# Kernel optimization log

Measured on AMD Instinct MI355X. Metric: run time of the kernel, lower is better.

## Reference

```python
import jax, jax.numpy as jnp
import numpy as np

C = 256
B, H, W = 16, 64, 64
CQK = C // 8


def setup_inputs() -> dict:
    key = jax.random.key(0)
    ks = jax.random.split(key, 8)
    s = 0.02
    return {
        "x": jax.random.normal(ks[0], (B, C, H, W), dtype=jnp.float32),
        "Wq": jax.random.normal(ks[1], (CQK, C), dtype=jnp.float32) * s,
        "bq": jax.random.normal(ks[2], (CQK,), dtype=jnp.float32) * s,
        "Wk": jax.random.normal(ks[3], (CQK, C), dtype=jnp.float32) * s,
        "bk": jax.random.normal(ks[4], (CQK,), dtype=jnp.float32) * s,
        "Wv": jax.random.normal(ks[5], (C, C), dtype=jnp.float32) * s,
        "bv": jax.random.normal(ks[6], (C,), dtype=jnp.float32) * s,
        "gamma": jax.random.normal(ks[7], (1,), dtype=jnp.float32) * 0.1,
    }


def reference(x, Wq, bq, Wk, bk, Wv, bv, gamma):
    b, c, h, w = x.shape
    n = h * w
    xf = x.reshape(b, c, n)  # flatten spatial -> tokens
    # 1x1 convs are per-token linear maps over channels
    q = jnp.einsum('oc,bcn->bon', Wq, xf) + bq[None, :, None]  # [B, C/8, N]
    k = jnp.einsum('oc,bcn->bon', Wk, xf) + bk[None, :, None]  # [B, C/8, N]
    v = jnp.einsum('oc,bcn->bon', Wv, xf) + bv[None, :, None]  # [B, C,   N]
    attn = jnp.einsum('bdi,bdj->bij', q, k)        # [B, N, N] = Q^T K
    attn = jax.nn.softmax(attn, axis=2)            # softmax over keys
    out = jnp.einsum('bcj,bij->bci', v, attn)      # V @ attn^T -> [B, C, N]
    out = out.reshape(b, c, h, w)
    return gamma[0] * out + x
```

## Files before the change

### kernel.cpp

```cpp
#include <hip/hip_runtime.h>
#include <hip/hip_bf16.h>

#define BB   16
#define CCH  256
#define DQK  32
#define NTOK 4096

typedef __attribute__((ext_vector_type(8)))  short short8;
typedef __attribute__((ext_vector_type(4)))  float f32x4;
typedef __attribute__((ext_vector_type(16))) float f32x16;
typedef unsigned short u16t;
typedef unsigned int   u32t;
typedef long long      i64t;

__device__ __forceinline__ u16t f2bf(float f){
  u32t u = __builtin_bit_cast(u32t, f);
  u += 0x7FFFu + ((u >> 16) & 1u);
  return (u16t)(u >> 16);
}
__device__ __forceinline__ u32t pk2(float a, float b){
  return (u32t)f2bf(a) | ((u32t)f2bf(b) << 16);
}
__device__ __forceinline__ void lane32swap(u32t& a, u32t& b){
  asm("v_permlane32_swap_b32 %0, %1" : "+v"(a), "+v"(b));
}
__device__ __forceinline__ float swapadd(float x){
  u32t a = __builtin_bit_cast(u32t, x), b = a;
  lane32swap(a, b);
  return __builtin_bit_cast(float, a) + __builtin_bit_cast(float, b);
}
__device__ __forceinline__ void gload16(const void* g, void* l){
  __builtin_amdgcn_global_load_lds(
      (const __attribute__((address_space(1))) void*)g,
      (__attribute__((address_space(3))) void*)l, 16, 0, 0);
}
__device__ __forceinline__ f32x16 zero16(){
  f32x16 z;
  #pragma unroll
  for (int i = 0; i < 16; ++i) z[i] = 0.f;
  return z;
}
#define mfma32(A, B, C)  __builtin_amdgcn_mfma_f32_32x32x16_bf16((A), (B), (C), 0, 0, 0)
#define mfma8(A, B, C)   __builtin_amdgcn_mfma_f32_32x32x16_fp8_fp8((A), (B), (C), 0, 0, 0)
__device__ __forceinline__ u32t pack4fp8(float a, float b, float c, float d){
  int t = __builtin_amdgcn_cvt_pk_fp8_f32(a, b, 0, false);
  t = __builtin_amdgcn_cvt_pk_fp8_f32(c, d, t, true);
  return (u32t)t;
}
__device__ __forceinline__ unsigned char tofp8(float v){
  return (unsigned char)(__builtin_amdgcn_cvt_pk_fp8_f32(v, 0.f, 0, false) & 0xFF);
}

__global__ __launch_bounds__(256) void k_wconv(const float* __restrict__ Wq,
    const float* __restrict__ Wk, const float* __restrict__ Wv,
    u16t* __restrict__ o){
  const int base = (blockIdx.x * 256 + threadIdx.x) * 4;
  float4 v;
  if (base < 8192)        v = *(const float4*)(Wq + base);
  else if (base < 16384)  v = *(const float4*)(Wk + base - 8192);
  else                    v = *(const float4*)(Wv + base - 16384);
  *(uint2*)(o + base) = make_uint2(pk2(v.x, v.y), pk2(v.z, v.w));
}

__global__ __launch_bounds__(256) void k_proj(const float* __restrict__ x,
    const u16t* __restrict__ Wb,
    const float* __restrict__ bq, const float* __restrict__ bk,
    const float* __restrict__ bv,
    u16t* __restrict__ Q, u16t* __restrict__ K, unsigned char* __restrict__ V){
  __shared__ __align__(16) u16t xt[32 * 512];
  const int b = blockIdx.y, nb = blockIdx.x * 64;
  const int tid = threadIdx.x;
  const int w = tid >> 6, lane = tid & 63;
  const int lo = lane & 15, g = lane >> 4;

  const float* xb = x + (size_t)b * CCH * NTOK + nb;
  const int cg = tid >> 4, n0 = (tid & 15) * 4;
  #pragma unroll
  for (int rep = 0; rep < 16; ++rep){
    const int c = rep * 16 + cg;
    float4 v = *(const float4*)(xb + (size_t)c * NTOK + n0);
    const int chunkb = (n0 >> 4) * 8 + (c >> 5);
    const int fl = 16 * ((c >> 3) & 3);
    const int e = c & 7;
    xt[chunkb * 512 + ((n0 & 15) + 0 + fl) * 8 + e] = f2bf(v.x);
    xt[chunkb * 512 + ((n0 & 15) + 1 + fl) * 8 + e] = f2bf(v.y);
    xt[chunkb * 512 + ((n0 & 15) + 2 + fl) * 8 + e] = f2bf(v.z);
    xt[chunkb * 512 + ((n0 & 15) + 3 + fl) * 8 + e] = f2bf(v.w);
  }
  __syncthreads();

  #pragma unroll
  for (int ot = 0; ot < 5; ++ot){
    const u16t* Wrow; const float* bias; int ob; int mode;
    if (ot == 0){
      if (w < 2){ Wrow = Wb;        bias = bq; ob = w * 16;       mode = 0; }
      else      { Wrow = Wb + 8192; bias = bk; ob = (w - 2) * 16; mode = 1; }
    } else { Wrow = Wb + 16384; bias = bv; ob = (ot - 1) * 64 + w * 16; mode = 2; }
    const u16t* wp = Wrow + (size_t)(ob + lo) * CCH + g * 8;

    f32x4 acc[4];
    #pragma unroll
    for (int s = 0; s < 4; ++s) acc[s] = (f32x4){0.f, 0.f, 0.f, 0.f};
    #pragma unroll
    for (int kc = 0; kc < CCH; kc += 32){
      const short8 af = *(const short8*)(wp + kc);
      #pragma unroll
      for (int s = 0; s < 4; ++s){
        const short8 bf = *(const short8*)(xt + (s * 8 + (kc >> 5)) * 512 + lane * 8);
        acc[s] = __builtin_amdgcn_mfma_f32_16x16x32_bf16(af, bf, acc[s], 0, 0, 0);
      }
    }
    #pragma unroll
    for (int s = 0; s < 4; ++s){
      #pragma unroll
      for (int r = 0; r < 4; ++r){
        const int o = ob + 4 * g + r;
        const int n = nb + s * 16 + lo;
        float val = acc[s][r] + bias[o];
        if (mode == 0){
          val *= 1.44269504088896f;
          Q[((size_t)b * NTOK + n) * DQK + o] = f2bf(val);
        } else if (mode == 1){
          K[((size_t)b * NTOK + n) * DQK + o] = f2bf(val);
        } else {
          const int swz = ((((s * 2) + (lo >> 3)) ^ ((o >> 1) & 7)) << 3) + (lo & 7);
          V[((size_t)b * CCH + o) * (size_t)NTOK + nb + swz] = tofp8(val);
        }
      }
    }
  }
}

__global__ __launch_bounds__(512, 4) void k_attn(
    const u16t* __restrict__ Q, const u16t* __restrict__ K,
    const unsigned char* __restrict__ V,
    const float* __restrict__ x, const float* __restrict__ gamma,
    float* __restrict__ out){
  __shared__ __align__(16) u16t KT[2 * 2048];
  __shared__ __align__(16) unsigned char Vt[2][16384];
  __shared__ __align__(16) unsigned char PT[2][8192];
  const int bid = blockIdx.x;
  const int b  = ((bid & 7) << 1) | ((bid >> 3) & 1);
  const int qt = bid >> 4;
  const int tid = threadIdx.x, w = tid >> 6, lane = tid & 63;
  const int qg = w & 3, ch = w >> 2;
  const int ql = lane & 31, hi = lane >> 5;
  const int qgb = qt * 128 + qg * 32;

  const u16t* Qb = Q + (size_t)b * NTOK * DQK;
  const u16t* Kb = K + (size_t)b * NTOK * DQK;
  const unsigned char* Vb = V + (size_t)b * CCH * NTOK;

  const short8 qf0 = *(const short8*)(Qb + (size_t)(qgb + ql) * DQK + hi * 8);
  const short8 qf1 = *(const short8*)(Qb + (size_t)(qgb + ql) * DQK + 16 + hi * 8);

  f32x16 acc[4];
  #pragma unroll
  for (int c = 0; c < 4; ++c) acc[c] = zero16();
  float l = 0.f;

  const char* vsrc0 = (const char*)Vb + (size_t)(w * 32 + (lane >> 2)) * NTOK + (lane & 3) * 16;
  const size_t kse = (size_t)((w & 1) * 32 + ql) * DQK + (w >> 1) * 16 + hi * 8;
  const char* ksrc0 = (const char*)Kb + kse * 2;
  const int kla = lane * 16;
  int vadd[4];
  #pragma unroll
  for (int kt = 0; kt < 4; ++kt)
    vadd[kt] = (ch * 128 + ql) * 64 + (((kt * 2 + hi) ^ ((ql >> 1) & 7)) << 3);
  const char* ldsV = (const char*)&Vt[0][0];
  const char* ldsK = (const char*)&KT[0];
  const char* ldsP = (const char*)&PT[0][0];
  char* ldsPw = (char*)&PT[0][0] + qg * 2048 + (ch * 2) * 512 + lane * 8;

  #define ESL(S, B) \
    { S[(B)+0] = __builtin_amdgcn_exp2f(S[(B)+0]); r0 += S[(B)+0]; \
      S[(B)+1] = __builtin_amdgcn_exp2f(S[(B)+1]); r1 += S[(B)+1]; \
      S[(B)+2] = __builtin_amdgcn_exp2f(S[(B)+2]); r2 += S[(B)+2]; \
      S[(B)+3] = __builtin_amdgcn_exp2f(S[(B)+3]); r3 += S[(B)+3]; }

  #define PVCHUNK(CS, VRD, EXPSLICE) \
    { const i64t vf0 = *(const i64t*)(ldsV + vadd[0] + (VRD)*16384 + (CS)*2048); \
      const i64t vf1 = *(const i64t*)(ldsV + vadd[1] + (VRD)*16384 + (CS)*2048); \
      const i64t vf2 = *(const i64t*)(ldsV + vadd[2] + (VRD)*16384 + (CS)*2048); \
      const i64t vf3 = *(const i64t*)(ldsV + vadd[3] + (VRD)*16384 + (CS)*2048); \
      acc[CS] = mfma8(vf0, pb0, acc[CS]); \
      acc[CS] = mfma8(vf1, pb1, acc[CS]); \
      acc[CS] = mfma8(vf2, pb2, acc[CS]); \
      acc[CS] = mfma8(vf3, pb3, acc[CS]); \
      EXPSLICE \
      __builtin_amdgcn_sched_group_barrier(0x100, 4, 0); \
      __builtin_amdgcn_sched_group_barrier(0x8,   4, 0); \
      __builtin_amdgcn_sched_group_barrier(0x2,   8, 0); }

  #define NOSL
  #define PBREADS(VRD) \
      const i64t pb0 = *(const i64t*)(ldsP + (VRD)*8192 + qg*2048 + 0*512 + lane*8); \
      const i64t pb1 = *(const i64t*)(ldsP + (VRD)*8192 + qg*2048 + 1*512 + lane*8); \
      const i64t pb2 = *(const i64t*)(ldsP + (VRD)*8192 + qg*2048 + 2*512 + lane*8); \
      const i64t pb3 = *(const i64t*)(ldsP + (VRD)*8192 + qg*2048 + 3*512 + lane*8);

  #define QKH(KRD, S) \
      { const char* kb_ = ldsK + (KRD)*4096 + ch*1024 + kla; \
        const short8 kfA = *(const short8*)(kb_); \
        const short8 kfB = *(const short8*)(kb_ + 2048); \
        S = mfma32(kfA, qf0, zero16()); \
        S = mfma32(kfB, qf1, S); }

  #define PWRITE(S, WB) \
      { u32t A1 = pack4fp8(S[0], S[1], S[2],  S[3]); \
        u32t B1 = pack4fp8(S[4], S[5], S[6],  S[7]); \
        lane32swap(A1, B1); \
        u32t A2 = pack4fp8(S[8], S[9], S[10], S[11]); \
        u32t B2 = pack4fp8(S[12], S[13], S[14], S[15]); \
        lane32swap(A2, B2); \
        *(i64t*)(ldsPw + (WB)*8192)       = __builtin_bit_cast(i64t, make_uint2(A1, B1)); \
        *(i64t*)(ldsPw + (WB)*8192 + 512) = __builtin_bit_cast(i64t, make_uint2(A2, B2)); }

  #define ABODY(T, VRD, KRD, KST) { \
      const int toff_ = ((T) + 1) * 64; \
      gload16(vsrc0 + toff_,                     &Vt[(VRD)^1][w * 2048]); \
      gload16(vsrc0 + (size_t)16 * NTOK + toff_, &Vt[(VRD)^1][w * 2048 + 1024]); \
      if (w < 4){ const int kt2_ = ((T) + 2 <= 63) ? (T) + 2 : 63; \
        gload16(ksrc0 + (size_t)kt2_ * 4096, &KT[(KST) * 2048 + w * 512]); } \
      PBREADS(VRD) \
      f32x16 s; \
      QKH(KRD, s) \
      float r0 = 0.f, r1 = 0.f, r2 = 0.f, r3 = 0.f; \
      PVCHUNK(0, VRD, ESL(s, 0)) \
      PVCHUNK(1, VRD, ESL(s, 4)) \
      PVCHUNK(2, VRD, ESL(s, 8)) \
      PVCHUNK(3, VRD, ESL(s, 12)) \
      l += (r0 + r1) + (r2 + r3); \
      PWRITE(s, (VRD)^1) \
      __syncthreads(); }

  gload16(vsrc0,                     &Vt[0][w * 2048]);
  gload16(vsrc0 + (size_t)16 * NTOK, &Vt[0][w * 2048 + 1024]);
  if (w < 4){
    gload16(ksrc0,        &KT[0 * 2048 + w * 512]);
    gload16(ksrc0 + 4096, &KT[1 * 2048 + w * 512]);
  }
  __syncthreads();

  {
    f32x16 s;
    QKH(0, s)
    float r0 = 0.f, r1 = 0.f, r2 = 0.f, r3 = 0.f;
    ESL(s, 0) ESL(s, 4) ESL(s, 8) ESL(s, 12)
    l = (r0 + r1) + (r2 + r3);
    PWRITE(s, 0)
  }
  __syncthreads();

  for (int t = 0; t < 62; t += 2){
    ABODY(t,     0, 1, 0)
    ABODY(t + 1, 1, 0, 1)
  }
  ABODY(62, 0, 1, 0)

  {
    PBREADS(1)
    PVCHUNK(0, 1, NOSL) PVCHUNK(1, 1, NOSL)
    PVCHUNK(2, 1, NOSL) PVCHUNK(3, 1, NOSL)
  }

  __syncthreads();
  const float lhalf = swapadd(l);
  float* lx = (float*)&PT[0][0];
  if (lane < 32) lx[(qg * 2 + ch) * 32 + ql] = lhalf;
  __syncthreads();
  const float lfull = lhalf + lx[(qg * 2 + (ch ^ 1)) * 32 + ql];
  const float inv = 1.0f / lfull;
  const float gm = gamma[0];
  const int n = qgb + ql;
  #pragma unroll
  for (int cs = 0; cs < 4; ++cs){
    #pragma unroll
    for (int r = 0; r < 16; ++r){
      const int c = ch * 128 + cs * 32 + (r & 3) + 8 * (r >> 2) + 4 * hi;
      const size_t idx = ((size_t)b * CCH + c) * NTOK + n;
      out[idx] = gm * (acc[cs][r] * inv) + x[idx];
    }
  }
  #undef ESL
  #undef PVCHUNK
  #undef NOSL
  #undef PBREADS
  #undef QKH
  #undef PWRITE
  #undef ABODY
}

extern "C" void kernel_launch(void* const* d_in, const int* in_sizes, int n_in,
                              void* d_out, int out_size, void* d_ws, size_t ws_size,
                              hipStream_t stream) {
  const float* x     = (const float*)d_in[0];
  const float* Wq    = (const float*)d_in[1];
  const float* bq    = (const float*)d_in[2];
  const float* Wk    = (const float*)d_in[3];
  const float* bk    = (const float*)d_in[4];
  const float* Wv    = (const float*)d_in[5];
  const float* bv    = (const float*)d_in[6];
  const float* gamma = (const float*)d_in[7];
  float* out = (float*)d_out;

  char* ws = (char*)d_ws;
  u16t* Qw = (u16t*)(ws);
  u16t* Kw = (u16t*)(ws + 4194304);
  unsigned char* Vw = (unsigned char*)(ws + 8388608);
  u16t* Wbf = (u16t*)d_out;

  hipLaunchKernelGGL(k_wconv, dim3(80), dim3(256), 0, stream, Wq, Wk, Wv, Wbf);
  hipLaunchKernelGGL(k_proj, dim3(NTOK / 64, BB), dim3(256), 0, stream,
                     x, Wbf, bq, bk, bv, Qw, Kw, Vw);
  hipLaunchKernelGGL(k_attn, dim3(512), dim3(512), 0, stream,
                     Qw, Kw, Vw, x, gamma, out);
}
```

Before: 163.6 us.

## Use 32x32x64 scaled MX fp8 MFMA for the PV product

Replaces four 32x32x16 fp8 MFMAs per channel chunk with one 32x32x64 scaled f8f6f4 MFMA, using unit scales. The V and P LDS read addressing and the P write layout are reworked to match the wider K-operand fragment, and the lane-swap shuffles in the P packing are dropped. The aim is to cut MFMA issue count and packing overhead in the attention inner loop. In exchange the P write/read pattern becomes 4-byte scattered accesses, which may cause more LDS traffic or bank conflicts.

```diff
diff --git a/kernel.cpp b/kernel.cpp
--- a/kernel.cpp
+++ b/kernel.cpp
@@ -7,6 +7,7 @@
 #define NTOK 4096
 
 typedef __attribute__((ext_vector_type(8)))  short short8;
+typedef __attribute__((ext_vector_type(8)))  int   i32x8;
 typedef __attribute__((ext_vector_type(4)))  float f32x4;
 typedef __attribute__((ext_vector_type(16))) float f32x16;
 typedef unsigned short u16t;
@@ -41,7 +42,7 @@
   return z;
 }
 #define mfma32(A, B, C)  __builtin_amdgcn_mfma_f32_32x32x16_bf16((A), (B), (C), 0, 0, 0)
-#define mfma8(A, B, C)   __builtin_amdgcn_mfma_f32_32x32x16_fp8_fp8((A), (B), (C), 0, 0, 0)
+#define mfmaMX(A, B, C)  __builtin_amdgcn_mfma_scale_f32_32x32x64_f8f6f4((A), (B), (C), 0, 0, 0, 127, 0, 127)
 __device__ __forceinline__ u32t pack4fp8(float a, float b, float c, float d){
   int t = __builtin_amdgcn_cvt_pk_fp8_f32(a, b, 0, false);
   t = __builtin_amdgcn_cvt_pk_fp8_f32(c, d, t, true);
@@ -163,14 +164,17 @@
   const size_t kse = (size_t)((w & 1) * 32 + ql) * DQK + (w >> 1) * 16 + hi * 8;
   const char* ksrc0 = (const char*)Kb + kse * 2;
   const int kla = lane * 16;
-  int vadd[4];
-  #pragma unroll
-  for (int kt = 0; kt < 4; ++kt)
-    vadd[kt] = (ch * 128 + ql) * 64 + (((kt * 2 + hi) ^ ((ql >> 1) & 7)) << 3);
+  int va[4];
+  #pragma unroll
+  for (int i = 0; i < 4; ++i){
+    const int c0 = ch * 128 + ql;
+    va[i] = (c0 & 127) * 64 + ch * 8192 + (((4 * hi + i) ^ ((c0 >> 1) & 7)) << 3);
+  }
   const char* ldsV = (const char*)&Vt[0][0];
   const char* ldsK = (const char*)&KT[0];
   const char* ldsP = (const char*)&PT[0][0];
-  char* ldsPw = (char*)&PT[0][0] + qg * 2048 + (ch * 2) * 512 + lane * 8;
+  char* ldsPw = (char*)&PT[0][0] + qg * 2048 + ch * 1024 + hi * 128 + ql * 4;
+  const int pread = qg * 2048 + hi * 1024 + ql * 4;
 
   #define ESL(S, B) \
     { S[(B)+0] = __builtin_amdgcn_exp2f(S[(B)+0]); r0 += S[(B)+0]; \
@@ -179,25 +183,25 @@
       S[(B)+3] = __builtin_amdgcn_exp2f(S[(B)+3]); r3 += S[(B)+3]; }
 
   #define PVCHUNK(CS, VRD, EXPSLICE) \
-    { const i64t vf0 = *(const i64t*)(ldsV + vadd[0] + (VRD)*16384 + (CS)*2048); \
-      const i64t vf1 = *(const i64t*)(ldsV + vadd[1] + (VRD)*16384 + (CS)*2048); \
-      const i64t vf2 = *(const i64t*)(ldsV + vadd[2] + (VRD)*16384 + (CS)*2048); \
-      const i64t vf3 = *(const i64t*)(ldsV + vadd[3] + (VRD)*16384 + (CS)*2048); \
-      acc[CS] = mfma8(vf0, pb0, acc[CS]); \
-      acc[CS] = mfma8(vf1, pb1, acc[CS]); \
-      acc[CS] = mfma8(vf2, pb2, acc[CS]); \
-      acc[CS] = mfma8(vf3, pb3, acc[CS]); \
+    { const uint2 v0 = *(const uint2*)(ldsV + va[0] + (VRD)*16384 + (CS)*2048); \
+      const uint2 v1 = *(const uint2*)(ldsV + va[1] + (VRD)*16384 + (CS)*2048); \
+      const uint2 v2 = *(const uint2*)(ldsV + va[2] + (VRD)*16384 + (CS)*2048); \
+      const uint2 v3 = *(const uint2*)(ldsV + va[3] + (VRD)*16384 + (CS)*2048); \
+      i32x8 av; \
+      av[0] = (int)v0.x; av[1] = (int)v0.y; av[2] = (int)v1.x; av[3] = (int)v1.y; \
+      av[4] = (int)v2.x; av[5] = (int)v2.y; av[6] = (int)v3.x; av[7] = (int)v3.y; \
+      acc[CS] = mfmaMX(av, pbv, acc[CS]); \
       EXPSLICE \
       __builtin_amdgcn_sched_group_barrier(0x100, 4, 0); \
-      __builtin_amdgcn_sched_group_barrier(0x8,   4, 0); \
+      __builtin_amdgcn_sched_group_barrier(0x8,   1, 0); \
       __builtin_amdgcn_sched_group_barrier(0x2,   8, 0); }
 
   #define NOSL
   #define PBREADS(VRD) \
-      const i64t pb0 = *(const i64t*)(ldsP + (VRD)*8192 + qg*2048 + 0*512 + lane*8); \
-      const i64t pb1 = *(const i64t*)(ldsP + (VRD)*8192 + qg*2048 + 1*512 + lane*8); \
-      const i64t pb2 = *(const i64t*)(ldsP + (VRD)*8192 + qg*2048 + 2*512 + lane*8); \
-      const i64t pb3 = *(const i64t*)(ldsP + (VRD)*8192 + qg*2048 + 3*512 + lane*8);
+      i32x8 pbv; \
+      _Pragma("unroll") \
+      for (int i_ = 0; i_ < 8; ++i_) \
+        pbv[i_] = *(const int*)(ldsP + (VRD)*8192 + pread + i_*128);
 
   #define QKH(KRD, S) \
       { const char* kb_ = ldsK + (KRD)*4096 + ch*1024 + kla; \
@@ -207,14 +211,10 @@
         S = mfma32(kfB, qf1, S); }
 
   #define PWRITE(S, WB) \
-      { u32t A1 = pack4fp8(S[0], S[1], S[2],  S[3]); \
-        u32t B1 = pack4fp8(S[4], S[5], S[6],  S[7]); \
-        lane32swap(A1, B1); \
-        u32t A2 = pack4fp8(S[8], S[9], S[10], S[11]); \
-        u32t B2 = pack4fp8(S[12], S[13], S[14], S[15]); \
-        lane32swap(A2, B2); \
-        *(i64t*)(ldsPw + (WB)*8192)       = __builtin_bit_cast(i64t, make_uint2(A1, B1)); \
-        *(i64t*)(ldsPw + (WB)*8192 + 512) = __builtin_bit_cast(i64t, make_uint2(A2, B2)); }
+      { *(u32t*)(ldsPw + (WB)*8192 +   0) = pack4fp8(S[0],  S[1],  S[2],  S[3]); \
+        *(u32t*)(ldsPw + (WB)*8192 + 256) = pack4fp8(S[4],  S[5],  S[6],  S[7]); \
+        *(u32t*)(ldsPw + (WB)*8192 + 512) = pack4fp8(S[8],  S[9],  S[10], S[11]); \
+        *(u32t*)(ldsPw + (WB)*8192 + 768) = pack4fp8(S[12], S[13], S[14], S[15]); }
 
   #define ABODY(T, VRD, KRD, KST) { \
       const int toff_ = ((T) + 1) * 64; \
```

New measurement: 579.8 us. 3.54x slower.

## Split attention work across 16 waves with producer and consumer roles

Applied to the files above, without the earlier changes.

Doubles the attention block to 1024 threads (16 waves). Eight producer waves compute QK^T, the exponentials and the P tiles, and also do PV over 64 channels. The other eight waves only do PV over their 64 channels. Each wave now holds half the accumulators, which lowers register pressure and raises parallelism per block. In exchange, block-wide barriers now span more waves and the producer and consumer waves carry unequal work. Launch bounds of (1024, 8) may force register spilling.

```diff
diff --git a/kernel.cpp b/kernel.cpp
--- a/kernel.cpp
+++ b/kernel.cpp
@@ -131,7 +131,7 @@
   }
 }
 
-__global__ __launch_bounds__(512, 4) void k_attn(
+__global__ __launch_bounds__(1024, 8) void k_attn(
     const u16t* __restrict__ Q, const u16t* __restrict__ K,
     const unsigned char* __restrict__ V,
     const float* __restrict__ x, const float* __restrict__ gamma,
@@ -143,7 +143,8 @@
   const int b  = ((bid & 7) << 1) | ((bid >> 3) & 1);
   const int qt = bid >> 4;
   const int tid = threadIdx.x, w = tid >> 6, lane = tid & 63;
-  const int qg = w & 3, ch = w >> 2;
+  const int qg = w & 3, cq = w >> 2;
+  const bool prod = (cq < 2);
   const int ql = lane & 31, hi = lane >> 5;
   const int qgb = qt * 128 + qg * 32;
 
@@ -151,26 +152,28 @@
   const u16t* Kb = K + (size_t)b * NTOK * DQK;
   const unsigned char* Vb = V + (size_t)b * CCH * NTOK;
 
-  const short8 qf0 = *(const short8*)(Qb + (size_t)(qgb + ql) * DQK + hi * 8);
-  const short8 qf1 = *(const short8*)(Qb + (size_t)(qgb + ql) * DQK + 16 + hi * 8);
-
-  f32x16 acc[4];
-  #pragma unroll
-  for (int c = 0; c < 4; ++c) acc[c] = zero16();
+  short8 qf0 = {}, qf1 = {};
+  if (prod){
+    qf0 = *(const short8*)(Qb + (size_t)(qgb + ql) * DQK + hi * 8);
+    qf1 = *(const short8*)(Qb + (size_t)(qgb + ql) * DQK + 16 + hi * 8);
+  }
+
+  f32x16 acc[2];
+  acc[0] = zero16(); acc[1] = zero16();
   float l = 0.f;
 
-  const char* vsrc0 = (const char*)Vb + (size_t)(w * 32 + (lane >> 2)) * NTOK + (lane & 3) * 16;
+  const char* vsrc0 = (const char*)Vb + (size_t)(w * 16 + (lane >> 2)) * NTOK + (lane & 3) * 16;
   const size_t kse = (size_t)((w & 1) * 32 + ql) * DQK + (w >> 1) * 16 + hi * 8;
   const char* ksrc0 = (const char*)Kb + kse * 2;
   const int kla = lane * 16;
   int vadd[4];
   #pragma unroll
   for (int kt = 0; kt < 4; ++kt)
-    vadd[kt] = (ch * 128 + ql) * 64 + (((kt * 2 + hi) ^ ((ql >> 1) & 7)) << 3);
+    vadd[kt] = (cq * 64 + ql) * 64 + (((kt * 2 + hi) ^ ((ql >> 1) & 7)) << 3);
   const char* ldsV = (const char*)&Vt[0][0];
   const char* ldsK = (const char*)&KT[0];
   const char* ldsP = (const char*)&PT[0][0];
-  char* ldsPw = (char*)&PT[0][0] + qg * 2048 + (ch * 2) * 512 + lane * 8;
+  char* ldsPw = (char*)&PT[0][0] + qg * 2048 + cq * 1024 + lane * 8;
 
   #define ESL(S, B) \
     { S[(B)+0] = __builtin_amdgcn_exp2f(S[(B)+0]); r0 += S[(B)+0]; \
@@ -200,7 +203,7 @@
       const i64t pb3 = *(const i64t*)(ldsP + (VRD)*8192 + qg*2048 + 3*512 + lane*8);
 
   #define QKH(KRD, S) \
-      { const char* kb_ = ldsK + (KRD)*4096 + ch*1024 + kla; \
+      { const char* kb_ = ldsK + (KRD)*4096 + cq*1024 + kla; \
         const short8 kfA = *(const short8*)(kb_); \
         const short8 kfB = *(const short8*)(kb_ + 2048); \
         S = mfma32(kfA, qf0, zero16()); \
@@ -218,31 +221,32 @@
 
   #define ABODY(T, VRD, KRD, KST) { \
       const int toff_ = ((T) + 1) * 64; \
-      gload16(vsrc0 + toff_,                     &Vt[(VRD)^1][w * 2048]); \
-      gload16(vsrc0 + (size_t)16 * NTOK + toff_, &Vt[(VRD)^1][w * 2048 + 1024]); \
+      gload16(vsrc0 + toff_, &Vt[(VRD)^1][w * 1024]); \
       if (w < 4){ const int kt2_ = ((T) + 2 <= 63) ? (T) + 2 : 63; \
         gload16(ksrc0 + (size_t)kt2_ * 4096, &KT[(KST) * 2048 + w * 512]); } \
       PBREADS(VRD) \
-      f32x16 s; \
-      QKH(KRD, s) \
-      float r0 = 0.f, r1 = 0.f, r2 = 0.f, r3 = 0.f; \
-      PVCHUNK(0, VRD, ESL(s, 0)) \
-      PVCHUNK(1, VRD, ESL(s, 4)) \
-      PVCHUNK(2, VRD, ESL(s, 8)) \
-      PVCHUNK(3, VRD, ESL(s, 12)) \
-      l += (r0 + r1) + (r2 + r3); \
-      PWRITE(s, (VRD)^1) \
+      if (prod){ \
+        f32x16 s; \
+        QKH(KRD, s) \
+        float r0 = 0.f, r1 = 0.f, r2 = 0.f, r3 = 0.f; \
+        PVCHUNK(0, VRD, ESL(s, 0) ESL(s, 4)) \
+        PVCHUNK(1, VRD, ESL(s, 8) ESL(s, 12)) \
+        l += (r0 + r1) + (r2 + r3); \
+        PWRITE(s, (VRD)^1) \
+      } else { \
+        PVCHUNK(0, VRD, NOSL) \
+        PVCHUNK(1, VRD, NOSL) \
+      } \
       __syncthreads(); }
 
-  gload16(vsrc0,                     &Vt[0][w * 2048]);
-  gload16(vsrc0 + (size_t)16 * NTOK, &Vt[0][w * 2048 + 1024]);
+  gload16(vsrc0, &Vt[0][w * 1024]);
   if (w < 4){
     gload16(ksrc0,        &KT[0 * 2048 + w * 512]);
     gload16(ksrc0 + 4096, &KT[1 * 2048 + w * 512]);
   }
   __syncthreads();
 
-  {
+  if (prod){
     f32x16 s;
     QKH(0, s)
     float r0 = 0.f, r1 = 0.f, r2 = 0.f, r3 = 0.f;
@@ -261,23 +265,24 @@
   {
     PBREADS(1)
     PVCHUNK(0, 1, NOSL) PVCHUNK(1, 1, NOSL)
-    PVCHUNK(2, 1, NOSL) PVCHUNK(3, 1, NOSL)
-  }
-
-  __syncthreads();
-  const float lhalf = swapadd(l);
+  }
+
+  __syncthreads();
   float* lx = (float*)&PT[0][0];
-  if (lane < 32) lx[(qg * 2 + ch) * 32 + ql] = lhalf;
-  __syncthreads();
-  const float lfull = lhalf + lx[(qg * 2 + (ch ^ 1)) * 32 + ql];
+  if (prod){
+    const float lhalf = swapadd(l);
+    if (lane < 32) lx[(qg * 2 + cq) * 32 + ql] = lhalf;
+  }
+  __syncthreads();
+  const float lfull = lx[(qg * 2 + 0) * 32 + ql] + lx[(qg * 2 + 1) * 32 + ql];
   const float inv = 1.0f / lfull;
   const float gm = gamma[0];
   const int n = qgb + ql;
   #pragma unroll
-  for (int cs = 0; cs < 4; ++cs){
+  for (int cs = 0; cs < 2; ++cs){
     #pragma unroll
     for (int r = 0; r < 16; ++r){
-      const int c = ch * 128 + cs * 32 + (r & 3) + 8 * (r >> 2) + 4 * hi;
+      const int c = cq * 64 + cs * 32 + (r & 3) + 8 * (r >> 2) + 4 * hi;
       const size_t idx = ((size_t)b * CCH + c) * NTOK + n;
       out[idx] = gm * (acc[cs][r] * inv) + x[idx];
     }
@@ -313,6 +318,6 @@
   hipLaunchKernelGGL(k_wconv, dim3(80), dim3(256), 0, stream, Wq, Wk, Wv, Wbf);
   hipLaunchKernelGGL(k_proj, dim3(NTOK / 64, BB), dim3(256), 0, stream,
                      x, Wbf, bq, bk, bv, Qw, Kw, Vw);
-  hipLaunchKernelGGL(k_attn, dim3(512), dim3(512), 0, stream,
+  hipLaunchKernelGGL(k_attn, dim3(512), dim3(1024), 0, stream,
                      Qw, Kw, Vw, x, gamma, out);
 }
```

Result: slower. 413.2 us (+152.5%).
